# Performance work log

Measured on AMD Instinct MI355X. Metric: run time of the kernel, lower is better.

## Reference

```python
import jax, jax.numpy as jnp
import numpy as np

N_NODES = 100000
N_EDGES = 1600000
D_IN = 128
D_OUT = 128
SLOPE = 0.2


def setup_inputs() -> dict:
    key = jax.random.key(0)
    k1, k2, k3, k4 = jax.random.split(key, 4)
    x = jax.random.normal(k1, (N_NODES, D_IN), dtype=jnp.float32)
    edge_index = jax.random.randint(k2, (2, N_EDGES), 0, N_NODES, dtype=jnp.int64)
    scale = 1.0 / np.sqrt(D_IN)
    W_l = jax.random.normal(k3, (D_OUT, D_IN), dtype=jnp.float32) * scale
    b_l = jnp.zeros((D_OUT,), dtype=jnp.float32)
    W_r = jax.random.normal(k4, (D_OUT, D_IN), dtype=jnp.float32) * scale
    return {"x": x, "edge_index": edge_index, "W_l": W_l, "b_l": b_l, "W_r": W_r}


def reference(x, edge_index, W_l, b_l, W_r):
    # SAGEConv with mean aggregation: out = lin_l(mean_{j in N(i)} x_j) + lin_r(x_i)
    src = edge_index[0]  # message sources (x_j)
    dst = edge_index[1]  # aggregation targets (node i)
    n = x.shape[0]
    msg = x[src]  # [E, D_IN] gather
    summed = jax.ops.segment_sum(msg, dst, num_segments=n)  # [N, D_IN]
    cnt = jax.ops.segment_sum(jnp.ones((src.shape[0],), x.dtype), dst, num_segments=n)
    agg = summed / jnp.maximum(cnt, 1.0)[:, None]  # mean; zero-degree -> 0
    out = agg @ W_l.T + b_l + x @ W_r.T  # lin_l has bias, lin_r bias=False (PyG)
    # LeakyReLU(slope); Dropout(0.5) is identity in eval mode
    return jnp.where(out > 0, out, SLOPE * out)
```

## Files before the change

kernel.cpp:

```cpp
#include <hip/hip_runtime.h>

#define D 128
#define N_SCAN 1024
#define BSH 7
#define MAXBINS 1024

typedef float  f32x4  __attribute__((ext_vector_type(4)));
typedef short  s16x8  __attribute__((ext_vector_type(8)));
typedef unsigned short us8 __attribute__((ext_vector_type(8)));

__device__ __forceinline__ unsigned short f2bf(float f) {
    unsigned b = __float_as_uint(f);
    return (unsigned short)((b + 0x7fffu + ((b >> 16) & 1u)) >> 16);
}
__device__ __forceinline__ float bf2f(unsigned short u) {
    return __uint_as_float((unsigned)u << 16);
}

__global__ __launch_bounds__(256) void bin_hist(
    const int* __restrict__ dst, int* __restrict__ bincnt, int E, int BINS)
{
    __shared__ int h[MAXBINS];
    for (int b = threadIdx.x; b < BINS; b += 256) h[b] = 0;
    __syncthreads();
    int base = blockIdx.x * 4096;
    #pragma unroll
    for (int j = 0; j < 16; ++j) {
        int e = base + j * 256 + threadIdx.x;
        if (e < E) atomicAdd(&h[dst[e] >> BSH], 1);
    }
    __syncthreads();
    for (int b = threadIdx.x; b < BINS; b += 256)
        if (h[b]) atomicAdd(&bincnt[b], h[b]);
}

__global__ __launch_bounds__(256) void bin_scan(
    const int* __restrict__ bincnt, int* __restrict__ binptr,
    int* __restrict__ binhead, int* __restrict__ rowptr,
    int BINS, int N, int E)
{
    __shared__ int sl[256];
    const int t = threadIdx.x;
    int v[4];
    int s = 0;
    #pragma unroll
    for (int j = 0; j < 4; ++j) {
        int i = t * 4 + j;
        int c = (i < BINS) ? bincnt[i] : 0;
        v[j] = s;
        s += c;
    }
    sl[t] = s;
    __syncthreads();
    for (int off = 1; off < 256; off <<= 1) {
        int add = (t >= off) ? sl[t - off] : 0;
        __syncthreads();
        sl[t] += add;
        __syncthreads();
    }
    int excl = sl[t] - s;
    #pragma unroll
    for (int j = 0; j < 4; ++j) {
        int i = t * 4 + j;
        if (i < BINS) { binptr[i] = excl + v[j]; binhead[i] = excl + v[j]; }
    }
    if (t == 0) { binptr[BINS] = E; rowptr[N] = E; }
}

__global__ __launch_bounds__(256) void partition_edges(
    const int* __restrict__ src, const int* __restrict__ dst,
    int* __restrict__ binhead, unsigned* __restrict__ packed_g, int E, int BINS)
{
    __shared__ int h[MAXBINS];
    __shared__ int goff[MAXBINS];
    __shared__ int fill[MAXBINS];
    const int t = threadIdx.x;
    for (int b = t; b < BINS; b += 256) { h[b] = 0; fill[b] = 0; }
    __syncthreads();
    int base = blockIdx.x * 4096;
    int eb[16];
    unsigned pk[16];
    #pragma unroll
    for (int j = 0; j < 16; ++j) {
        int e = base + j * 256 + t;
        if (e < E) {
            int d = dst[e], s = src[e];
            eb[j] = d >> BSH;
            pk[j] = ((unsigned)(d & ((1 << BSH) - 1)) << 17) | (unsigned)s;
            atomicAdd(&h[eb[j]], 1);
        } else eb[j] = -1;
    }
    __syncthreads();
    for (int b = t; b < BINS; b += 256)
        if (h[b]) goff[b] = atomicAdd(&binhead[b], h[b]);
    __syncthreads();
    #pragma unroll
    for (int j = 0; j < 16; ++j) {
        if (eb[j] >= 0) {
            int p = goff[eb[j]] + atomicAdd(&fill[eb[j]], 1);
            packed_g[p] = pk[j];
        }
    }
}

__global__ __launch_bounds__(256) void bin_finalize(
    const unsigned* __restrict__ packed_g, const int* __restrict__ binptr,
    int* __restrict__ rowptr, int* __restrict__ srcs, int N)
{
    const int bin = blockIdx.x, t = threadIdx.x;
    const int beg = binptr[bin], end = binptr[bin + 1];
    const int node0 = bin << BSH;
    __shared__ int c[128];
    __shared__ int pf[128];
    __shared__ int hd[128];
    if (t < 128) c[t] = 0;
    __syncthreads();
    for (int i = beg + t; i < end; i += 256)
        atomicAdd(&c[packed_g[i] >> 17], 1);
    __syncthreads();
    if (t < 128) pf[t] = c[t];
    __syncthreads();
    for (int off = 1; off < 128; off <<= 1) {
        int v = 0;
        if (t < 128 && t >= off) v = pf[t - off];
        __syncthreads();
        if (t < 128) pf[t] += v;
        __syncthreads();
    }
    if (t < 128) {
        int node = node0 + t;
        if (node < N) {
            int r = beg + pf[t] - c[t];
            rowptr[node] = r;
            hd[t] = r;
        }
    }
    __syncthreads();
    for (int i = beg + t; i < end; i += 256) {
        unsigned p = packed_g[i];
        int dl = p >> 17;
        int s = p & 0x1FFFF;
        int pos = atomicAdd(&hd[dl], 1);
        srcs[pos] = s;
    }
}

__global__ __launch_bounds__(256) void hist_kernel(
    const int* __restrict__ dst, int* __restrict__ cnt, int E)
{
    int e = blockIdx.x * 256 + threadIdx.x;
    if (e < E) atomicAdd(&cnt[dst[e]], 1);
}

__global__ __launch_bounds__(256) void scan1_kernel(
    const int* __restrict__ cnt, int* __restrict__ rowptr,
    int* __restrict__ blocksum, int N)
{
    __shared__ int sl[256];
    const int t = threadIdx.x;
    const int base = blockIdx.x * N_SCAN + t * 4;
    int v[4];
    int s = 0;
    #pragma unroll
    for (int j = 0; j < 4; ++j) {
        int i = base + j;
        int c = (i < N) ? cnt[i] : 0;
        v[j] = s;
        s += c;
    }
    sl[t] = s;
    __syncthreads();
    for (int off = 1; off < 256; off <<= 1) {
        int add = (t >= off) ? sl[t - off] : 0;
        __syncthreads();
        sl[t] += add;
        __syncthreads();
    }
    int incl = sl[t];
    int excl = incl - s;
    #pragma unroll
    for (int j = 0; j < 4; ++j) {
        int i = base + j;
        if (i < N) rowptr[i] = excl + v[j];
    }
    if (t == 255) blocksum[blockIdx.x] = incl;
}

__global__ void scan2_kernel(const int* __restrict__ blocksum,
                             int* __restrict__ blockoff, int nblk)
{
    if (threadIdx.x == 0 && blockIdx.x == 0) {
        int s = 0;
        for (int b = 0; b < nblk; ++b) { blockoff[b] = s; s += blocksum[b]; }
    }
}

__global__ __launch_bounds__(256) void scan3_kernel(
    int* __restrict__ rowptr, const int* __restrict__ blockoff,
    int* __restrict__ head, int N, int E)
{
    int i = blockIdx.x * 256 + threadIdx.x;
    if (i < N) {
        int r = rowptr[i] + blockoff[i >> 10];
        rowptr[i] = r;
        head[i] = r;
    } else if (i == N) {
        rowptr[N] = E;
    }
}

__global__ __launch_bounds__(256) void scatter_edges(
    const int* __restrict__ src, const int* __restrict__ dst,
    int* __restrict__ head, int* __restrict__ srcs, int E)
{
    int e = blockIdx.x * 256 + threadIdx.x;
    if (e < E) {
        int pos = atomicAdd(&head[dst[e]], 1);
        srcs[pos] = src[e];
    }
}

__global__ __launch_bounds__(256) void convert_bf16(
    const float* __restrict__ x, unsigned short* __restrict__ xb, long long total)
{
    long long i = ((long long)blockIdx.x * 256 + threadIdx.x) * 8;
    if (i >= total) return;
    float4 f0 = *(const float4*)(x + i);
    float4 f1 = *(const float4*)(x + i + 4);
    us8 u;
    u[0] = f2bf(f0.x); u[1] = f2bf(f0.y); u[2] = f2bf(f0.z); u[3] = f2bf(f0.w);
    u[4] = f2bf(f1.x); u[5] = f2bf(f1.y); u[6] = f2bf(f1.z); u[7] = f2bf(f1.w);
    *(us8*)(xb + i) = u;
}

__global__ __launch_bounds__(256) void aggregate_bf16(
    const unsigned short* __restrict__ xb, const int* __restrict__ rowptr,
    const int* __restrict__ srcs, unsigned short* __restrict__ aggb, int N)
{
    int wid  = (blockIdx.x * 256 + threadIdx.x) >> 6;
    int lane = threadIdx.x & 63;
    if (wid >= N) return;
    int beg = rowptr[wid], end = rowptr[wid + 1];
    const int q  = lane >> 4;
    const int sl = lane & 15;

    float acc[8] = {};
    int e = beg;
    for (; e + 8 <= end; e += 8) {
        int s0 = srcs[e + q];
        int s1 = srcs[e + 4 + q];
        us8 v0 = *(const us8*)(xb + (long long)s0 * D + sl * 8);
        us8 v1 = *(const us8*)(xb + (long long)s1 * D + sl * 8);
        #pragma unroll
        for (int j = 0; j < 8; ++j) acc[j] += bf2f(v0[j]);
        #pragma unroll
        for (int j = 0; j < 8; ++j) acc[j] += bf2f(v1[j]);
    }
    for (; e < end; e += 4) {
        int ee = e + q;
        if (ee < end) {
            int s0 = srcs[ee];
            us8 v0 = *(const us8*)(xb + (long long)s0 * D + sl * 8);
            #pragma unroll
            for (int j = 0; j < 8; ++j) acc[j] += bf2f(v0[j]);
        }
    }
    #pragma unroll
    for (int j = 0; j < 8; ++j) {
        acc[j] += __shfl_xor(acc[j], 16, 64);
        acc[j] += __shfl_xor(acc[j], 32, 64);
    }
    float inv = 1.0f / fmaxf((float)(end - beg), 1.0f);
    if (q == 0) {
        us8 u;
        #pragma unroll
        for (int j = 0; j < 8; ++j) u[j] = f2bf(acc[j] * inv);
        *(us8*)(aggb + (long long)wid * D + sl * 8) = u;
    }
}

__global__ __launch_bounds__(256) void mm_mfma(
    const unsigned short* __restrict__ xb,
    const unsigned short* __restrict__ aggb,
    const float* __restrict__ Wl, const float* __restrict__ bl,
    const float* __restrict__ Wr,
    float* __restrict__ out, int N)
{
    __shared__ char wlds[64 * 1024];
    const int tid = threadIdx.x;

    for (int c = tid; c < 4096; c += 256) {
        int byte = c * 16;
        int o  = byte >> 9;
        int k2 = (byte & 511) >> 1;
        const float* srcw = (k2 < 128) ? (Wl + o * D + k2) : (Wr + o * D + (k2 - 128));
        float4 f0 = *(const float4*)(srcw);
        float4 f1 = *(const float4*)(srcw + 4);
        us8 u;
        u[0] = f2bf(f0.x); u[1] = f2bf(f0.y); u[2] = f2bf(f0.z); u[3] = f2bf(f0.w);
        u[4] = f2bf(f1.x); u[5] = f2bf(f1.y); u[6] = f2bf(f1.z); u[7] = f2bf(f1.w);
        *(us8*)(wlds + (byte ^ ((o & 7) << 4))) = u;
    }
    __syncthreads();

    const int lane = tid & 63;
    const int wv   = tid >> 6;
    const long long m0 = (long long)blockIdx.x * 64 + wv * 16;
    const int arow = lane & 15;
    const int kq   = lane >> 4;
    const long long mrow = m0 + arow;
    const bool valid = (mrow < N);
    const unsigned short* aP = aggb + mrow * D + kq * 8;
    const unsigned short* xP = xb   + mrow * D + kq * 8;

    f32x4 acc[8] = {};

    #pragma unroll
    for (int s = 0; s < 8; ++s) {
        s16x8 afrag = {0, 0, 0, 0, 0, 0, 0, 0};
        if (valid) {
            const unsigned short* ap = (s < 4) ? (aP + s * 32) : (xP + (s - 4) * 32);
            afrag = *(const s16x8*)ap;
        }
        #pragma unroll
        for (int t = 0; t < 8; ++t) {
            int o = t * 16 + arow;
            int boff = (o << 9) + s * 64 + kq * 16;
            boff ^= (o & 7) << 4;
            s16x8 bfrag = *(const s16x8*)(wlds + boff);
            acc[t] = __builtin_amdgcn_mfma_f32_16x16x32_bf16(afrag, bfrag, acc[t], 0, 0, 0);
        }
    }

    const int crow = (lane >> 4) * 4;
    const int ccol = lane & 15;
    #pragma unroll
    for (int t = 0; t < 8; ++t) {
        int col = t * 16 + ccol;
        float bb = bl[col];
        #pragma unroll
        for (int r = 0; r < 4; ++r) {
            long long row = m0 + crow + r;
            if (row < N) {
                float v = acc[t][r] + bb;
                out[row * D + col] = v > 0.f ? v : 0.2f * v;
            }
        }
    }
}

__global__ __launch_bounds__(256) void aggregate_f32(
    const float* __restrict__ x, const int* __restrict__ rowptr,
    const int* __restrict__ srcs, float* __restrict__ out, int N)
{
    int wid  = (blockIdx.x * 256 + threadIdx.x) >> 6;
    int lane = threadIdx.x & 63;
    if (wid >= N) return;
    int beg = rowptr[wid], end = rowptr[wid + 1];
    const float2* x2 = (const float2*)x;
    float ax = 0.f, ay = 0.f;
    int e = beg;
    for (; e + 4 <= end; e += 4) {
        int s0 = srcs[e], s1 = srcs[e + 1], s2 = srcs[e + 2], s3 = srcs[e + 3];
        float2 v0 = x2[(long long)s0 * 64 + lane];
        float2 v1 = x2[(long long)s1 * 64 + lane];
        float2 v2 = x2[(long long)s2 * 64 + lane];
        float2 v3 = x2[(long long)s3 * 64 + lane];
        ax += v0.x + v1.x + v2.x + v3.x;
        ay += v0.y + v1.y + v2.y + v3.y;
    }
    for (; e < end; ++e) {
        float2 v = x2[(long long)srcs[e] * 64 + lane];
        ax += v.x; ay += v.y;
    }
    float inv = 1.0f / fmaxf((float)(end - beg), 1.0f);
    float2 o; o.x = ax * inv; o.y = ay * inv;
    ((float2*)out)[(long long)wid * 64 + lane] = o;
}

#define MT 32
#define KT 32
__global__ __launch_bounds__(256) void sage_mm_f32(
    const float* __restrict__ x, const float* __restrict__ Wl,
    const float* __restrict__ bl, const float* __restrict__ Wr,
    float* __restrict__ out, int N)
{
    __shared__ __align__(16) float a_s[KT][MT + 4];
    __shared__ __align__(16) float x_s[KT][MT + 4];
    __shared__ __align__(16) float wl_s[KT][D + 4];
    __shared__ __align__(16) float wr_s[KT][D + 4];

    const int tid = threadIdx.x;
    const int tx = tid & 31;
    const int ty = tid >> 5;
    const int node0 = blockIdx.x * MT;

    float acc[4][4] = {};

    for (int k0 = 0; k0 < D; k0 += KT) {
        __syncthreads();
        for (int i = tid; i < MT * KT; i += 256) {
            int n = i >> 5, kk = i & 31;
            int node = node0 + n;
            float av = 0.f, xv = 0.f;
            if (node < N) {
                av = out[(long long)node * D + k0 + kk];
                xv = x[(long long)node * D + k0 + kk];
            }
            a_s[kk][n] = av;
            x_s[kk][n] = xv;
        }
        for (int i = tid; i < D * KT; i += 256) {
            int o = i >> 5, kk = i & 31;
            wl_s[kk][o] = Wl[o * D + k0 + kk];
            wr_s[kk][o] = Wr[o * D + k0 + kk];
        }
        __syncthreads();
        #pragma unroll
        for (int kk = 0; kk < KT; ++kk) {
            float4 a4 = *(const float4*)&a_s[kk][ty * 4];
            float4 x4 = *(const float4*)&x_s[kk][ty * 4];
            float4 l4 = *(const float4*)&wl_s[kk][tx * 4];
            float4 r4 = *(const float4*)&wr_s[kk][tx * 4];
            float an[4] = {a4.x, a4.y, a4.z, a4.w};
            float xn[4] = {x4.x, x4.y, x4.z, x4.w};
            float lo[4] = {l4.x, l4.y, l4.z, l4.w};
            float ro[4] = {r4.x, r4.y, r4.z, r4.w};
            #pragma unroll
            for (int n = 0; n < 4; ++n)
                #pragma unroll
                for (int o = 0; o < 4; ++o)
                    acc[n][o] += an[n] * lo[o] + xn[n] * ro[o];
        }
    }

    float4 b4 = *(const float4*)&bl[tx * 4];
    float bb[4] = {b4.x, b4.y, b4.z, b4.w};
    #pragma unroll
    for (int n = 0; n < 4; ++n) {
        int node = node0 + ty * 4 + n;
        if (node < N) {
            float4 o4;
            float* po = (float*)&o4;
            #pragma unroll
            for (int o = 0; o < 4; ++o) {
                float v = acc[n][o] + bb[o];
                po[o] = v > 0.f ? v : 0.2f * v;
            }
            *(float4*)&out[(long long)node * D + tx * 4] = o4;
        }
    }
}

extern "C" void kernel_launch(void* const* d_in, const int* in_sizes, int n_in,
                              void* d_out, int out_size, void* d_ws, size_t ws_size,
                              hipStream_t stream)
{
    const float* x  = (const float*)d_in[0];
    const int*   ei = (const int*)d_in[1];
    const float* Wl = (const float*)d_in[2];
    const float* bl = (const float*)d_in[3];
    const float* Wr = (const float*)d_in[4];

    const int E = in_sizes[1] / 2;
    const int N = out_size / D;
    const int* src = ei;
    const int* dst = ei + E;
    float* out = (float*)d_out;
    const int BINS = (N + (1 << BSH) - 1) >> BSH;

    size_t off = 0;
    auto take = [&](size_t bytes) { size_t p = off; off = (off + bytes + 255) & ~(size_t)255; return p; };
    char* w = (char*)d_ws;
    int* rowptr   = (int*)(w + take((size_t)(N + 1) * 4));
    int* srcs     = (int*)(w + take((size_t)E * 4));
    int* bincnt   = (int*)(w + take((size_t)BINS * 4));
    int* binptr   = (int*)(w + take((size_t)(BINS + 1) * 4));
    int* binhead  = (int*)(w + take((size_t)BINS * 4));
    int* blocksum = (int*)(w + take(4096));
    int* blockoff = (int*)(w + take(4096));
    unsigned* packed = (unsigned*)(w + take((size_t)E * 4));
    size_t binned_base = off;
    unsigned short* xbf   = (unsigned short*)(w + take((size_t)N * D * 2));
    unsigned short* aggbf = (unsigned short*)(w + take((size_t)N * D * 2));
    size_t full_needed = off;

    const bool binned_ok = (BINS <= MAXBINS) && (N < (1 << 17)) && (ws_size >= full_needed);

    if (binned_ok) {
        hipMemsetAsync(bincnt, 0, (size_t)BINS * 4, stream);
        int pb = (E + 4095) / 4096;
        bin_hist<<<pb, 256, 0, stream>>>(dst, bincnt, E, BINS);
        bin_scan<<<1, 256, 0, stream>>>(bincnt, binptr, binhead, rowptr, BINS, N, E);
        partition_edges<<<pb, 256, 0, stream>>>(src, dst, binhead, packed, E, BINS);
        bin_finalize<<<BINS, 256, 0, stream>>>(packed, binptr, rowptr, srcs, N);

        long long total = (long long)N * D;
        int cb = (int)((total / 8 + 255) / 256);
        convert_bf16<<<cb, 256, 0, stream>>>(x, xbf, total);
        int ab = (N * 64 + 255) / 256;
        aggregate_bf16<<<ab, 256, 0, stream>>>(xbf, rowptr, srcs, aggbf, N);
        int mb = (N + 63) / 64;
        mm_mfma<<<mb, 256, 0, stream>>>(xbf, aggbf, Wl, bl, Wr, out, N);
        return;
    }

    off = 0;
    int* cnt    = (int*)(w + take((size_t)N * 4));
    rowptr      = (int*)(w + take((size_t)(N + 1) * 4));
    int* head   = (int*)(w + take((size_t)N * 4));
    blocksum    = (int*)(w + take(4096));
    blockoff    = (int*)(w + take(4096));
    srcs        = (int*)(w + take((size_t)E * 4));
    size_t base_needed = off;
    xbf   = (unsigned short*)(w + take((size_t)N * D * 2));
    aggbf = (unsigned short*)(w + take((size_t)N * D * 2));
    size_t bf16_needed = off;

    hipMemsetAsync(cnt, 0, (size_t)N * 4, stream);
    const int eb = (E + 255) / 256;
    hist_kernel<<<eb, 256, 0, stream>>>(dst, cnt, E);
    const int nblk = (N + N_SCAN - 1) / N_SCAN;
    scan1_kernel<<<nblk, 256, 0, stream>>>(cnt, rowptr, blocksum, N);
    scan2_kernel<<<1, 64, 0, stream>>>(blocksum, blockoff, nblk);
    scan3_kernel<<<(N + 1 + 255) / 256, 256, 0, stream>>>(rowptr, blockoff, head, N, E);
    scatter_edges<<<eb, 256, 0, stream>>>(src, dst, head, srcs, E);

    if (ws_size >= bf16_needed) {
        long long total = (long long)N * D;
        int cb = (int)((total / 8 + 255) / 256);
        convert_bf16<<<cb, 256, 0, stream>>>(x, xbf, total);
        int ab = (N * 64 + 255) / 256;
        aggregate_bf16<<<ab, 256, 0, stream>>>(xbf, rowptr, srcs, aggbf, N);
        int mb = (N + 63) / 64;
        mm_mfma<<<mb, 256, 0, stream>>>(xbf, aggbf, Wl, bl, Wr, out, N);
    } else {
        (void)base_needed; (void)binned_base;
        int ab = (N * 64 + 255) / 256;
        aggregate_f32<<<ab, 256, 0, stream>>>(x, rowptr, srcs, out, N);
        sage_mm_f32<<<(N + MT - 1) / MT, 256, 0, stream>>>(x, Wl, bl, Wr, out, N);
    }
}
```

Baseline: 187.5 us.

## Pre-convert weights to swizzled bf16 once and enlarge GEMM tiles to 256 rows

Adds a small kernel that converts W_l and W_r to bf16 in the swizzled LDS layout once per call and stores them in workspace. A new GEMM kernel copies that 64KB image straight into LDS and processes 256 rows per 512-thread block instead of 64. This removes the per-block float-to-bf16 weight conversion and cuts the number of weight reloads by four. The cost is an extra launch and fewer, larger blocks, which may lower occupancy.

```diff
diff --git a/kernel.cpp b/kernel.cpp
--- a/kernel.cpp
+++ b/kernel.cpp
@@ -276,6 +276,98 @@
         #pragma unroll
         for (int j = 0; j < 8; ++j) u[j] = f2bf(acc[j] * inv);
         *(us8*)(aggb + (long long)wid * D + sl * 8) = u;
+    }
+}
+
+__global__ __launch_bounds__(256) void convert_w(
+    const float* __restrict__ Wl, const float* __restrict__ Wr,
+    unsigned short* __restrict__ wbf)
+{
+    int c = blockIdx.x * 256 + threadIdx.x;
+    if (c >= 4096) return;
+    int byte = c * 16;
+    int o  = byte >> 9;
+    int k2 = (byte & 511) >> 1;
+    const float* srcw = (k2 < 128) ? (Wl + o * D + k2) : (Wr + o * D + (k2 - 128));
+    float4 f0 = *(const float4*)(srcw);
+    float4 f1 = *(const float4*)(srcw + 4);
+    us8 u;
+    u[0] = f2bf(f0.x); u[1] = f2bf(f0.y); u[2] = f2bf(f0.z); u[3] = f2bf(f0.w);
+    u[4] = f2bf(f1.x); u[5] = f2bf(f1.y); u[6] = f2bf(f1.z); u[7] = f2bf(f1.w);
+    *(us8*)((char*)wbf + (byte ^ ((o & 7) << 4))) = u;
+}
+
+__global__ __launch_bounds__(512) void mm_mfma2(
+    const unsigned short* __restrict__ xb,
+    const unsigned short* __restrict__ aggb,
+    const unsigned short* __restrict__ wbf,
+    const float* __restrict__ bl,
+    float* __restrict__ out, int N)
+{
+    __shared__ char wlds[64 * 1024];
+    const int tid = threadIdx.x;
+
+    {
+        const us8* s = (const us8*)wbf;
+        us8* d = (us8*)wlds;
+        #pragma unroll
+        for (int j = 0; j < 8; ++j)
+            d[j * 512 + tid] = s[j * 512 + tid];
+    }
+    __syncthreads();
+
+    const int lane = tid & 63;
+    const int wv   = tid >> 6;
+    const long long m0 = (long long)blockIdx.x * 256 + wv * 32;
+    const int arow = lane & 15;
+    const int kq   = lane >> 4;
+    const long long r0 = m0 + arow;
+    const long long r1 = m0 + 16 + arow;
+    const bool v0 = (r0 < N), v1 = (r1 < N);
+    const unsigned short* a0 = aggb + r0 * D + kq * 8;
+    const unsigned short* x0 = xb   + r0 * D + kq * 8;
+    const unsigned short* a1 = aggb + r1 * D + kq * 8;
+    const unsigned short* x1 = xb   + r1 * D + kq * 8;
+
+    f32x4 acc0[8] = {};
+    f32x4 acc1[8] = {};
+
+    #pragma unroll
+    for (int s = 0; s < 8; ++s) {
+        s16x8 af0 = {0, 0, 0, 0, 0, 0, 0, 0};
+        s16x8 af1 = {0, 0, 0, 0, 0, 0, 0, 0};
+        if (v0) af0 = *(const s16x8*)((s < 4) ? (a0 + s * 32) : (x0 + (s - 4) * 32));
+        if (v1) af1 = *(const s16x8*)((s < 4) ? (a1 + s * 32) : (x1 + (s - 4) * 32));
+        #pragma unroll
+        for (int t = 0; t < 8; ++t) {
+            int o = t * 16 + arow;
+            int boff = (o << 9) + s * 64 + kq * 16;
+            boff ^= (o & 7) << 4;
+            s16x8 bf = *(const s16x8*)(wlds + boff);
+            acc0[t] = __builtin_amdgcn_mfma_f32_16x16x32_bf16(af0, bf, acc0[t], 0, 0, 0);
+            acc1[t] = __builtin_amdgcn_mfma_f32_16x16x32_bf16(af1, bf, acc1[t], 0, 0, 0);
+        }
+    }
+
+    const int crow = (lane >> 4) * 4;
+    const int ccol = lane & 15;
+    #pragma unroll
+    for (int t = 0; t < 8; ++t) {
+        int col = t * 16 + ccol;
+        float bb = bl[col];
+        #pragma unroll
+        for (int r = 0; r < 4; ++r) {
+            long long row0 = m0 + crow + r;
+            if (row0 < N) {
+                float vv = acc0[t][r] + bb;
+                out[row0 * D + col] = vv > 0.f ? vv : 0.2f * vv;
+            }
+            long long row1 = m0 + 16 + crow + r;
+            if (row1 < N) {
+                float vv = acc1[t][r] + bb;
+                out[row1 * D + col] = vv > 0.f ? vv : 0.2f * vv;
+            }
+        }
     }
 }
 
@@ -477,10 +569,8 @@
     int* bincnt   = (int*)(w + take((size_t)BINS * 4));
     int* binptr   = (int*)(w + take((size_t)(BINS + 1) * 4));
     int* binhead  = (int*)(w + take((size_t)BINS * 4));
-    int* blocksum = (int*)(w + take(4096));
-    int* blockoff = (int*)(w + take(4096));
     unsigned* packed = (unsigned*)(w + take((size_t)E * 4));
-    size_t binned_base = off;
+    unsigned short* wbf = (unsigned short*)(w + take(64 * 1024));
     unsigned short* xbf   = (unsigned short*)(w + take((size_t)N * D * 2));
     unsigned short* aggbf = (unsigned short*)(w + take((size_t)N * D * 2));
     size_t full_needed = off;
@@ -488,6 +578,8 @@
     const bool binned_ok = (BINS <= MAXBINS) && (N < (1 << 17)) && (ws_size >= full_needed);
 
     if (binned_ok) {
+        convert_w<<<16, 256, 0, stream>>>(Wl, Wr, wbf);
+
         hipMemsetAsync(bincnt, 0, (size_t)BINS * 4, stream);
         int pb = (E + 4095) / 4096;
         bin_hist<<<pb, 256, 0, stream>>>(dst, bincnt, E, BINS);
@@ -500,8 +592,8 @@
         convert_bf16<<<cb, 256, 0, stream>>>(x, xbf, total);
         int ab = (N * 64 + 255) / 256;
         aggregate_bf16<<<ab, 256, 0, stream>>>(xbf, rowptr, srcs, aggbf, N);
-        int mb = (N + 63) / 64;
-        mm_mfma<<<mb, 256, 0, stream>>>(xbf, aggbf, Wl, bl, Wr, out, N);
+        int mb = (N + 255) / 256;
+        mm_mfma2<<<mb, 512, 0, stream>>>(xbf, aggbf, wbf, bl, out, N);
         return;
     }
 
@@ -509,8 +601,8 @@
     int* cnt    = (int*)(w + take((size_t)N * 4));
     rowptr      = (int*)(w + take((size_t)(N + 1) * 4));
     int* head   = (int*)(w + take((size_t)N * 4));
-    blocksum    = (int*)(w + take(4096));
-    blockoff    = (int*)(w + take(4096));
+    int* blocksum = (int*)(w + take(4096));
+    int* blockoff = (int*)(w + take(4096));
     srcs        = (int*)(w + take((size_t)E * 4));
     size_t base_needed = off;
     xbf   = (unsigned short*)(w + take((size_t)N * D * 2));
@@ -535,7 +627,7 @@
         int mb = (N + 63) / 64;
         mm_mfma<<<mb, 256, 0, stream>>>(xbf, aggbf, Wl, bl, Wr, out, N);
     } else {
-        (void)base_needed; (void)binned_base;
+        (void)base_needed;
         int ab = (N * 64 + 255) / 256;
         aggregate_f32<<<ab, 256, 0, stream>>>(x, rowptr, srcs, out, N);
         sage_mm_f32<<<(N + MT - 1) / MT, 256, 0, stream>>>(x, Wl, bl, Wr, out, N);
```

Result: faster. 165.4 us (-11.8%).
